# Kernel optimization log

Measured on AMD Instinct MI355X. Metric: run time of the kernel, lower is better.

The kernel has to match this reference:

```python
import jax, jax.numpy as jnp
import numpy as np

ALPHA = 1.0
BETA = 0.25
NUM_EMBEDS = 8192
EMBED_DIM = 512
B, T = 32, 256


def setup_inputs() -> dict:
    key = jax.random.key(0)
    k1, k2 = jax.random.split(key)
    z_e = jax.random.normal(k1, (B, EMBED_DIM, T), dtype=jnp.float32)
    codebook = jax.random.normal(k2, (NUM_EMBEDS, EMBED_DIM), dtype=jnp.float32)
    return {"z_e": z_e, "codebook": codebook}


def reference(z_e, codebook):
    # z_e: (b, d, t) -> (b, t, d)
    z = jnp.transpose(z_e, (0, 2, 1))
    b, t, d = z.shape
    flat = z.reshape(-1, d)  # (N, d), N = b*t

    # squared euclidean distances to every codebook vector: (N, K)
    dists = (
        jnp.sum(flat * flat, axis=1, keepdims=True)
        + jnp.sum(codebook * codebook, axis=1)
        - 2.0 * flat @ codebook.T
    )
    idx = jnp.argmin(dists, axis=1)  # (N,)

    # codebook lookup (equivalent to one-hot @ codebook)
    z_q = codebook[idx].reshape(b, t, d)

    # commitment loss (codebook is EMA-updated, so only e_latent term)
    e_latent_loss = jnp.mean((jax.lax.stop_gradient(z_q) - z) ** 2)
    vq_loss = ALPHA * BETA * e_latent_loss

    # straight-through estimator
    z_q_st = z + jax.lax.stop_gradient(z_q - z)
    z_q_out = jnp.transpose(z_q_st, (0, 2, 1))  # back to (b, d, t)

    # perplexity from mean one-hot assignment probabilities
    counts = jnp.zeros((codebook.shape[0],), dtype=jnp.float32).at[idx].add(1.0)
    avg_probs = counts / flat.shape[0]
    perplexity = jnp.exp(-jnp.sum(avg_probs * jnp.log(avg_probs + 1e-10)))

    return z_q_out, vq_loss, perplexity
```

## Files before the change

kernel.cpp:

```cpp
#include <hip/hip_runtime.h>
#include <stdint.h>

typedef _Float16 half8 __attribute__((ext_vector_type(8)));
typedef float floatx16 __attribute__((ext_vector_type(16)));
typedef unsigned long long u64;

#define ALPHA_ 1.0f
#define BETA_ 0.25f
#define NUM_EMBEDS 8192
#define EMBED_DIM 512
#define B_ 32
#define T_ 256
#define N_TOK 8192
#define MAXPAIRS (1 << 20)


__device__ __forceinline__ uint32_t mono(float s) {
    uint32_t u = __float_as_uint(s);
    return (u & 0x80000000u) ? ~u : (u | 0x80000000u);
}
__device__ __forceinline__ float unmono(uint32_t v) {
    return __uint_as_float((v & 0x80000000u) ? (v ^ 0x80000000u) : ~v);
}

__global__ void pack_cb_kernel(const float* __restrict__ cb, _Float16* __restrict__ cf,
                               float* __restrict__ cnorm, unsigned int* __restrict__ maxC2) {
    int row = blockIdx.x * 4 + (threadIdx.x >> 6);
    int l = threadIdx.x & 63;
    const float* src = cb + (size_t)row * EMBED_DIM + l * 8;
    float4 v0 = *(const float4*)src;
    float4 v1 = *(const float4*)(src + 4);
    float x[8] = {v0.x, v0.y, v0.z, v0.w, v1.x, v1.y, v1.z, v1.w};
    half8 hh;
    float s = 0.f;
#pragma unroll
    for (int j = 0; j < 8; ++j) {
        s += x[j] * x[j];
        hh[j] = (_Float16)x[j];
    }
    int slot = (l >> 2) * 2 + ((l >> 1) & 1);
    int flane = (row & 31) + (l & 1) * 32;
    *(half8*)(cf + (size_t)(row >> 5) * 16384 + (size_t)slot * 512 + flane * 8) = hh;
#pragma unroll
    for (int d = 32; d; d >>= 1) s += __shfl_xor(s, d, 64);
    if (l == 0) {
        cnorm[row] = s;
        atomicMax(maxC2, __float_as_uint(s));
    }
}

__global__ void pack_z_kernel(const float* __restrict__ z, _Float16* __restrict__ zf,
                              float* __restrict__ znorm) {
    int tid = threadIdx.x;
    int l = tid & 63, ds = tid >> 6;
    int n = blockIdx.x * 64 + l;
    int b = n >> 8, t = n & 255;
    int kk = ds >> 1, hfb = ds & 1;
    int tb = n >> 7, q = (n >> 5) & 3;
    size_t lanebase = (size_t)tb * 65536 + (size_t)q * 512 +
                      (size_t)((n & 31) + hfb * 32) * 8;
    float zz = 0.f;
    const int g0 = blockIdx.y * 4;
    for (int g = g0; g < g0 + 4; ++g) {
        int d0 = g * 32 + ds * 8;
        const float* src = z + ((size_t)b * EMBED_DIM + d0) * T_ + t;
        half8 hh;
#pragma unroll
        for (int j = 0; j < 8; ++j) {
            float zo = src[(size_t)j * T_];
            zz += zo * zo;
            hh[j] = (_Float16)(-2.0f * zo);
        }
        int slot = g * 2 + kk;
        *(half8*)(zf + lanebase + (size_t)slot * 2048) = hh;
    }
    atomicAdd(&znorm[n], zz);
}

#define MFMA16(a, b, c) __builtin_amdgcn_mfma_f32_32x32x16_f16(a, b, c, 0, 0, 0)

#define LDSET(s, hs)                                                  \
    fr[s][0] = *(const half8*)(Ab0 + (hs) * 512 + l8);                \
    fr[s][1] = *(const half8*)(Ab1 + (hs) * 512 + l8);                \
    fr[s][2] = *(const half8*)(Bb + (hs) * 2048 + 0 * 512 + l8);      \
    fr[s][3] = *(const half8*)(Bb + (hs) * 2048 + 1 * 512 + l8);      \
    fr[s][4] = *(const half8*)(Bb + (hs) * 2048 + 2 * 512 + l8);      \
    fr[s][5] = *(const half8*)(Bb + (hs) * 2048 + 3 * 512 + l8);

__global__ __launch_bounds__(256, 2) void argmin_kernel(
    const _Float16* __restrict__ cb_h, const _Float16* __restrict__ zt_h,
    const float* __restrict__ cnorm, u64* __restrict__ slot_m1,
    _Float16* __restrict__ slot_d) {
    const int tid = threadIdx.x;
    const int l = tid & 63;
    const int wv = tid >> 6;
    const int l31 = l & 31;
    const int hf = l >> 5;
    const int cid = blockIdx.y * 4 + wv;
    const _Float16* Ab0 = cb_h + (size_t)(cid * 2) * 16384;
    const _Float16* Ab1 = Ab0 + 16384;
    const _Float16* Bb = zt_h + (size_t)blockIdx.x * 65536;
    const int l8 = l * 8;

    floatx16 acc[2][4];
#pragma unroll
    for (int a = 0; a < 2; ++a)
#pragma unroll
        for (int q = 0; q < 4; ++q)
#pragma unroll
            for (int r = 0; r < 16; ++r) acc[a][q][r] = 0.f;

    half8 fr[3][6];
    LDSET(0, 0)
    LDSET(1, 1)
#pragma unroll
    for (int t = 0; t < 32; ++t) {
        const int s = t % 3;
        if ((t & 1) == 0) __syncthreads();
        if (t + 2 < 32) {
            LDSET((t + 2) % 3, t + 2)
        }
#pragma unroll
        for (int q = 0; q < 4; ++q) acc[0][q] = MFMA16(fr[s][0], fr[s][2 + q], acc[0][q]);
#pragma unroll
        for (int q = 0; q < 4; ++q) acc[1][q] = MFMA16(fr[s][1], fr[s][2 + q], acc[1][q]);
    }

    const int cb0 = cid * 64;
#pragma unroll
    for (int q = 0; q < 4; ++q) {
        u64 m1k = ~0ULL;
        float m1v = 3.4e38f, m2 = 3.4e38f;
#pragma unroll
        for (int ti = 0; ti < 2; ++ti)
#pragma unroll
            for (int g = 0; g < 4; ++g) {
                const int cb4 = cb0 + ti * 32 + g * 8 + hf * 4;
                float4 cn = *(const float4*)(cnorm + cb4);
                float sv[4] = {cn.x + acc[ti][q][g * 4 + 0], cn.y + acc[ti][q][g * 4 + 1],
                               cn.z + acc[ti][q][g * 4 + 2], cn.w + acc[ti][q][g * 4 + 3]};
#pragma unroll
                for (int r = 0; r < 4; ++r) {
                    u64 key = ((u64)mono(sv[r]) << 32) | (uint32_t)(cb4 + r);
                    if (key < m1k) { m2 = m1v; m1v = sv[r]; m1k = key; }
                    else m2 = fminf(m2, sv[r]);
                }
            }
        u64 ok = __shfl_xor(m1k, 32, 64);
        float ov = __shfl_xor(m1v, 32, 64);
        float om2 = __shfl_xor(m2, 32, 64);
        if (ok < m1k) { m2 = fminf(fminf(m2, om2), m1v); m1v = ov; m1k = ok; }
        else m2 = fminf(fminf(m2, om2), ov);
        if (hf == 0) {
            int tok = blockIdx.x * 128 + q * 32 + l31;
            slot_m1[((size_t)cid << 13) + tok] = m1k;
            slot_d[((size_t)cid << 13) + tok] = (_Float16)(m2 - m1v);
        }
    }
}

__global__ void combine_kernel(const u64* __restrict__ slot_m1, const _Float16* __restrict__ slot_d,
                               const float* __restrict__ znorm, const unsigned int* __restrict__ maxC2,
                               u64* __restrict__ wexact, int* __restrict__ pairs,
                               int* __restrict__ npairs) {
    int tid = threadIdx.x;
    int tok = blockIdx.x * 16 + (tid >> 4);
    int sub = tid & 15;
    u64 g1 = ~0ULL;
    float g1v = 3.4e38f, g2 = 3.4e38f;
    for (int c = sub; c < 128; c += 16) {
        u64 k = slot_m1[((size_t)c << 13) + tok];
        float kv = unmono((uint32_t)(k >> 32));
        float v2 = kv + (float)slot_d[((size_t)c << 13) + tok];
        if (k < g1) { g2 = fminf(g2, g1v); g1 = k; g1v = kv; }
        else g2 = fminf(g2, kv);
        g2 = fminf(g2, v2);
    }
#pragma unroll
    for (int m = 1; m < 16; m <<= 1) {
        u64 ok = __shfl_xor(g1, m, 64);
        float ov = __shfl_xor(g1v, m, 64);
        float o2 = __shfl_xor(g2, m, 64);
        if (ok < g1) { g2 = fminf(fminf(g2, o2), g1v); g1 = ok; g1v = ov; }
        else g2 = fminf(fminf(g2, o2), ov);
    }
    float maxC = sqrtf(__uint_as_float(*maxC2));
    float thr = sqrtf(znorm[tok]) * maxC * (1.0f / 256.0f) + 0.15f;
    if (g2 - g1v > thr) {
        if (sub == 0) wexact[tok] = g1;
    } else {
        float cutv = g1v + thr;
        for (int c = sub; c < 128; c += 16) {
            u64 k = slot_m1[((size_t)c << 13) + tok];
            if (unmono((uint32_t)(k >> 32)) <= cutv) {
                int i = atomicAdd(npairs, 1);
                if (i < MAXPAIRS) pairs[i] = (tok << 7) | c;
            }
        }
    }
}

__global__ void fallback_kernel(const float* __restrict__ z, const float* __restrict__ cb,
                                const float* __restrict__ cnorm,
                                const int* __restrict__ pairs, const int* __restrict__ npairs,
                                u64* __restrict__ wexact) {
    __shared__ float zs[4][512];
    int n = *npairs;
    if (n > MAXPAIRS) n = MAXPAIRS;
    const int l = threadIdx.x & 63, wv = threadIdx.x >> 6;
    int wid = blockIdx.x * 4 + wv;
    const int wstride = gridDim.x * 4;
    for (int pi = wid; pi < n; pi += wstride) {
        int pk = pairs[pi];
        int tok = pk >> 7, cid = pk & 127;
        int b = tok >> 8, t = tok & 255;
        const float* zp = z + (size_t)b * EMBED_DIM * T_ + t;
        float zv[8];
#pragma unroll
        for (int j = 0; j < 8; ++j) zv[j] = zp[(size_t)(l * 8 + j) * T_];
        *(float4*)&zs[wv][l * 8] = make_float4(zv[0], zv[1], zv[2], zv[3]);
        *(float4*)&zs[wv][l * 8 + 4] = make_float4(zv[4], zv[5], zv[6], zv[7]);
        int code = cid * 64 + l;
        const float* cp = cb + (size_t)code * EMBED_DIM;
        float acc = 0.f;
#pragma unroll 4
        for (int d = 0; d < 512; d += 4) {
            float4 cv = *(const float4*)(cp + d);
            float4 zq = *(const float4*)&zs[wv][d];
            acc += cv.x * zq.x + cv.y * zq.y + cv.z * zq.z + cv.w * zq.w;
        }
        float s = cnorm[code] - 2.0f * acc;
        u64 key = ((u64)mono(s) << 32) | (uint32_t)code;
#pragma unroll
        for (int m = 32; m; m >>= 1) {
            u64 ok = __shfl_xor(key, m, 64);
            key = ok < key ? ok : key;
        }
        if (l == 0) atomicMin(&wexact[tok], key);
    }
}

__global__ void gather_kernel(const float* __restrict__ z, const float* __restrict__ cb,
                              const u64* __restrict__ wexact,
                              float* __restrict__ out, int* __restrict__ counts,
                              float* __restrict__ sse_acc) {
    __shared__ unsigned int sIdx[32];
    __shared__ float red[16];
    const int tid = threadIdx.x;
    const int n0 = blockIdx.x * 32;
    const int b = n0 >> 8;
    const int t0 = n0 & 255;
    if (tid < 32) {
        unsigned int idx = (unsigned int)(wexact[n0 + tid] & 0xffffffffULL);
        sIdx[tid] = idx;
        atomicAdd(&counts[idx], 1);
    }
    __syncthreads();
    const int sg = tid >> 5;
    const int l32 = tid & 31;
    const float* crow = cb + (size_t)sIdx[l32] * EMBED_DIM;
    const size_t base = ((size_t)b * EMBED_DIM) * T_ + (size_t)(t0 + l32);
    float sse = 0.f;
    const int d0 = sg * 32;
#pragma unroll 8
    for (int i = 0; i < 32; ++i) {
        int d = d0 + i;
        float v = crow[d];
        size_t o = base + (size_t)d * T_;
        float diff = v - z[o];
        out[o] = v;
        sse += diff * diff;
    }
#pragma unroll
    for (int m = 16; m; m >>= 1) sse += __shfl_xor(sse, m, 64);
    if (l32 == 0) red[sg] = sse;
    __syncthreads();
    if (tid == 0) {
        float s = 0.f;
#pragma unroll
        for (int i = 0; i < 16; ++i) s += red[i];
        atomicAdd(sse_acc, s);
    }
}

__global__ void finalize_kernel(const int* __restrict__ counts,
                                const float* __restrict__ sse_acc,
                                float* __restrict__ out) {
    __shared__ float red[4];
    const int tid = threadIdx.x;
    float e = 0.f;
    for (int k = tid; k < NUM_EMBEDS; k += 256) {
        float p = (float)counts[k] * (1.0f / (float)N_TOK);
        e += p * logf(p + 1e-10f);
    }
    for (int m = 32; m; m >>= 1) e += __shfl_xor(e, m, 64);
    if ((tid & 63) == 0) red[tid >> 6] = e;
    __syncthreads();
    if (tid == 0) {
        float ent = red[0] + red[1] + red[2] + red[3];
        size_t off = (size_t)B_ * EMBED_DIM * T_;
        out[off + 0] = (ALPHA_ * BETA_) * sse_acc[0] / (float)((size_t)N_TOK * EMBED_DIM);
        out[off + 1] = expf(-ent);
    }
}

extern "C" void kernel_launch(void* const* d_in, const int* in_sizes, int n_in,
                              void* d_out, int out_size, void* d_ws, size_t ws_size,
                              hipStream_t stream) {
    const float* z = (const float*)d_in[0];
    const float* cb = (const float*)d_in[1];
    float* out = (float*)d_out;
    char* ws = (char*)d_ws;
    u64* wexact = (u64*)ws;
    float* cnorm = (float*)(ws + 65536);
    int* counts = (int*)(ws + 98304);
    float* znorm = (float*)(ws + 131072);
    float* sse = (float*)(ws + 163840);
    int* npairs = (int*)(ws + 163844);
    unsigned int* maxC2 = (unsigned int*)(ws + 163848);
    u64* slot_m1 = (u64*)(ws + (1ull << 20));
    _Float16* slot_d = (_Float16*)(ws + (9ull << 20));
    _Float16* cb_h = (_Float16*)(ws + (10ull << 20));
    _Float16* zt_h = (_Float16*)(ws + (18ull << 20));
    int* pairs = (int*)(ws + (26ull << 20));

    hipMemsetAsync(wexact, 0xFF, NUM_EMBEDS * sizeof(u64), stream);
    hipMemsetAsync(counts, 0, 65536 + 12, stream);

    pack_cb_kernel<<<NUM_EMBEDS / 4, 256, 0, stream>>>(cb, cb_h, cnorm, maxC2);
    pack_z_kernel<<<dim3(N_TOK / 64, 4), 256, 0, stream>>>(z, zt_h, znorm);
    argmin_kernel<<<dim3(N_TOK / 128, 32), 256, 0, stream>>>(cb_h, zt_h, cnorm, slot_m1, slot_d);
    combine_kernel<<<N_TOK / 16, 256, 0, stream>>>(slot_m1, slot_d, znorm, maxC2, wexact, pairs, npairs);
    fallback_kernel<<<512, 256, 0, stream>>>(z, cb, cnorm, pairs, npairs, wexact);
    gather_kernel<<<N_TOK / 32, 512, 0, stream>>>(z, cb, wexact, out, counts, sse);
    finalize_kernel<<<1, 256, 0, stream>>>(counts, sse, out);
}
```

Measured before the change: 426.3 us.

## Stage argmin GEMM tiles through LDS, widen code tiles, fuse pack and fallback kernels

Result: slower. 516.9 us (+21.2%).

```diff
diff --git a/kernel.cpp b/kernel.cpp
--- a/kernel.cpp
+++ b/kernel.cpp
@@ -12,7 +12,6 @@
 #define B_ 32
 #define T_ 256
 #define N_TOK 8192
-#define MAXPAIRS (1 << 20)
 
 
 __device__ __forceinline__ uint32_t mono(float s) {
@@ -23,116 +22,152 @@
     return __uint_as_float((v & 0x80000000u) ? (v ^ 0x80000000u) : ~v);
 }
 
-__global__ void pack_cb_kernel(const float* __restrict__ cb, _Float16* __restrict__ cf,
-                               float* __restrict__ cnorm, unsigned int* __restrict__ maxC2) {
-    int row = blockIdx.x * 4 + (threadIdx.x >> 6);
-    int l = threadIdx.x & 63;
-    const float* src = cb + (size_t)row * EMBED_DIM + l * 8;
-    float4 v0 = *(const float4*)src;
-    float4 v1 = *(const float4*)(src + 4);
-    float x[8] = {v0.x, v0.y, v0.z, v0.w, v1.x, v1.y, v1.z, v1.w};
-    half8 hh;
-    float s = 0.f;
-#pragma unroll
-    for (int j = 0; j < 8; ++j) {
-        s += x[j] * x[j];
-        hh[j] = (_Float16)x[j];
-    }
-    int slot = (l >> 2) * 2 + ((l >> 1) & 1);
-    int flane = (row & 31) + (l & 1) * 32;
-    *(half8*)(cf + (size_t)(row >> 5) * 16384 + (size_t)slot * 512 + flane * 8) = hh;
-#pragma unroll
-    for (int d = 32; d; d >>= 1) s += __shfl_xor(s, d, 64);
-    if (l == 0) {
-        cnorm[row] = s;
-        atomicMax(maxC2, __float_as_uint(s));
-    }
-}
-
-__global__ void pack_z_kernel(const float* __restrict__ z, _Float16* __restrict__ zf,
-                              float* __restrict__ znorm) {
+__global__ void pack_kernel(const float* __restrict__ cb, const float* __restrict__ z,
+                            _Float16* __restrict__ cf, _Float16* __restrict__ zf,
+                            float* __restrict__ cnorm, unsigned int* __restrict__ maxC2,
+                            float* __restrict__ znorm) {
     int tid = threadIdx.x;
-    int l = tid & 63, ds = tid >> 6;
-    int n = blockIdx.x * 64 + l;
-    int b = n >> 8, t = n & 255;
-    int kk = ds >> 1, hfb = ds & 1;
-    int tb = n >> 7, q = (n >> 5) & 3;
-    size_t lanebase = (size_t)tb * 65536 + (size_t)q * 512 +
-                      (size_t)((n & 31) + hfb * 32) * 8;
-    float zz = 0.f;
-    const int g0 = blockIdx.y * 4;
-    for (int g = g0; g < g0 + 4; ++g) {
-        int d0 = g * 32 + ds * 8;
-        const float* src = z + ((size_t)b * EMBED_DIM + d0) * T_ + t;
+    if (blockIdx.x < 2048) {
+        int row = blockIdx.x * 4 + (tid >> 6);
+        int l = tid & 63;
+        const float* src = cb + (size_t)row * EMBED_DIM + l * 8;
+        float4 v0 = *(const float4*)src;
+        float4 v1 = *(const float4*)(src + 4);
+        float x[8] = {v0.x, v0.y, v0.z, v0.w, v1.x, v1.y, v1.z, v1.w};
         half8 hh;
+        float s = 0.f;
 #pragma unroll
         for (int j = 0; j < 8; ++j) {
-            float zo = src[(size_t)j * T_];
-            zz += zo * zo;
-            hh[j] = (_Float16)(-2.0f * zo);
-        }
-        int slot = g * 2 + kk;
-        *(half8*)(zf + lanebase + (size_t)slot * 2048) = hh;
-    }
-    atomicAdd(&znorm[n], zz);
+            s += x[j] * x[j];
+            hh[j] = (_Float16)x[j];
+        }
+        int slot = (l >> 2) * 2 + ((l >> 1) & 1);
+        int flane = (row & 31) + (l & 1) * 32;
+        *(half8*)(cf + (size_t)(row >> 5) * 16384 + (size_t)slot * 512 + flane * 8) = hh;
+#pragma unroll
+        for (int d = 32; d; d >>= 1) s += __shfl_xor(s, d, 64);
+        if (l == 0) {
+            cnorm[row] = s;
+            atomicMax(maxC2, __float_as_uint(s));
+        }
+    } else {
+        int zb = blockIdx.x - 2048;
+        int bx = zb & 127, g0 = (zb >> 7) * 4;
+        int l = tid & 63, ds = tid >> 6;
+        int n = bx * 64 + l;
+        int b = n >> 8, t = n & 255;
+        int kk = ds >> 1, hfb = ds & 1;
+        int tb = n >> 7, q = (n >> 5) & 3;
+        size_t lanebase = (size_t)tb * 65536 + (size_t)q * 512 +
+                          (size_t)((n & 31) + hfb * 32) * 8;
+        float zz = 0.f;
+        for (int g = g0; g < g0 + 4; ++g) {
+            int d0 = g * 32 + ds * 8;
+            const float* src = z + ((size_t)b * EMBED_DIM + d0) * T_ + t;
+            half8 hh;
+#pragma unroll
+            for (int j = 0; j < 8; ++j) {
+                float zo = src[(size_t)j * T_];
+                zz += zo * zo;
+                hh[j] = (_Float16)(-2.0f * zo);
+            }
+            int slot = g * 2 + kk;
+            *(half8*)(zf + lanebase + (size_t)slot * 2048) = hh;
+        }
+        atomicAdd(&znorm[n], zz);
+    }
 }
 
 #define MFMA16(a, b, c) __builtin_amdgcn_mfma_f32_32x32x16_f16(a, b, c, 0, 0, 0)
-
-#define LDSET(s, hs)                                                  \
-    fr[s][0] = *(const half8*)(Ab0 + (hs) * 512 + l8);                \
-    fr[s][1] = *(const half8*)(Ab1 + (hs) * 512 + l8);                \
-    fr[s][2] = *(const half8*)(Bb + (hs) * 2048 + 0 * 512 + l8);      \
-    fr[s][3] = *(const half8*)(Bb + (hs) * 2048 + 1 * 512 + l8);      \
-    fr[s][4] = *(const half8*)(Bb + (hs) * 2048 + 2 * 512 + l8);      \
-    fr[s][5] = *(const half8*)(Bb + (hs) * 2048 + 3 * 512 + l8);
 
 __global__ __launch_bounds__(256, 2) void argmin_kernel(
     const _Float16* __restrict__ cb_h, const _Float16* __restrict__ zt_h,
     const float* __restrict__ cnorm, u64* __restrict__ slot_m1,
     _Float16* __restrict__ slot_d) {
+    __shared__ alignas(16) _Float16 Sm[2][12288];
     const int tid = threadIdx.x;
     const int l = tid & 63;
     const int wv = tid >> 6;
     const int l31 = l & 31;
     const int hf = l >> 5;
-    const int cid = blockIdx.y * 4 + wv;
-    const _Float16* Ab0 = cb_h + (size_t)(cid * 2) * 16384;
-    const _Float16* Ab1 = Ab0 + 16384;
-    const _Float16* Bb = zt_h + (size_t)blockIdx.x * 65536;
+    const int wm = wv >> 1;
+    const int wn = wv & 1;
     const int l8 = l * 8;
 
-    floatx16 acc[2][4];
-#pragma unroll
-    for (int a = 0; a < 2; ++a)
-#pragma unroll
-        for (int q = 0; q < 4; ++q)
+    const int flat = blockIdx.y * gridDim.x + blockIdx.x;
+    const int cpx = (gridDim.x * gridDim.y) >> 3;
+    const int swz = (flat & 7) * cpx + (flat >> 3);
+    const int tb = swz & 63;
+    const int cg = swz >> 6;
+    const int c0 = cg * 256;
+
+    const _Float16* Abase = cb_h + (size_t)(cg * 8) * 16384;
+    const _Float16* Bbase = zt_h + (size_t)tb * 65536;
+
+    floatx16 acc[4][2];
+#pragma unroll
+    for (int a = 0; a < 4; ++a)
+#pragma unroll
+        for (int q = 0; q < 2; ++q)
 #pragma unroll
             for (int r = 0; r < 16; ++r) acc[a][q][r] = 0.f;
 
-    half8 fr[3][6];
-    LDSET(0, 0)
-    LDSET(1, 1)
-#pragma unroll
-    for (int t = 0; t < 32; ++t) {
-        const int s = t % 3;
-        if ((t & 1) == 0) __syncthreads();
-        if (t + 2 < 32) {
-            LDSET((t + 2) % 3, t + 2)
-        }
-#pragma unroll
-        for (int q = 0; q < 4; ++q) acc[0][q] = MFMA16(fr[s][0], fr[s][2 + q], acc[0][q]);
-#pragma unroll
-        for (int q = 0; q < 4; ++q) acc[1][q] = MFMA16(fr[s][1], fr[s][2 + q], acc[1][q]);
-    }
-
-    const int cb0 = cid * 64;
-#pragma unroll
-    for (int q = 0; q < 4; ++q) {
+    half8 sa[4], sb[2];
+    auto load_stage = [&](int t) {
+#pragma unroll
+        for (int i = 0; i < 4; ++i) {
+            int j = wv * 4 + i;
+            sa[i] = *(const half8*)(Abase + (size_t)(j >> 1) * 16384 +
+                                    (size_t)(2 * t + (j & 1)) * 512 + l8);
+        }
+#pragma unroll
+        for (int i = 0; i < 2; ++i) {
+            int jb = wv * 2 + i;
+            sb[i] = *(const half8*)(Bbase + (size_t)(2 * t + (jb >> 2)) * 2048 +
+                                    (size_t)(jb & 3) * 512 + l8);
+        }
+    };
+    auto write_stage = [&](int p) {
+        _Float16* dst = Sm[p];
+#pragma unroll
+        for (int i = 0; i < 4; ++i)
+            *(half8*)(dst + (wv * 4 + i) * 512 + l8) = sa[i];
+#pragma unroll
+        for (int i = 0; i < 2; ++i)
+            *(half8*)(dst + 8192 + (wv * 2 + i) * 512 + l8) = sb[i];
+    };
+
+    load_stage(0);
+    write_stage(0);
+    __syncthreads();
+    for (int t = 0; t < 16; ++t) {
+        const int p = t & 1;
+        if (t < 15) load_stage(t + 1);
+        const _Float16* Ab = Sm[p] + (size_t)(wm * 8) * 512;
+        const _Float16* Bb = Sm[p] + 8192 + (size_t)wn * 1024;
+#pragma unroll
+        for (int kk = 0; kk < 2; ++kk) {
+            half8 b0 = *(const half8*)(Bb + kk * 2048 + l8);
+            half8 b1 = *(const half8*)(Bb + kk * 2048 + 512 + l8);
+#pragma unroll
+            for (int ti = 0; ti < 4; ++ti) {
+                half8 a = *(const half8*)(Ab + (size_t)(ti * 2 + kk) * 512 + l8);
+                acc[ti][0] = MFMA16(a, b0, acc[ti][0]);
+                acc[ti][1] = MFMA16(a, b1, acc[ti][1]);
+            }
+        }
+        if (t < 15) write_stage(p ^ 1);
+        __syncthreads();
+    }
+
+    const int cb0 = c0 + wm * 128;
+    const int cid = cg * 2 + wm;
+#pragma unroll
+    for (int q = 0; q < 2; ++q) {
         u64 m1k = ~0ULL;
         float m1v = 3.4e38f, m2 = 3.4e38f;
 #pragma unroll
-        for (int ti = 0; ti < 2; ++ti)
+        for (int ti = 0; ti < 4; ++ti)
 #pragma unroll
             for (int g = 0; g < 4; ++g) {
                 const int cb4 = cb0 + ti * 32 + g * 8 + hf * 4;
@@ -152,23 +187,29 @@
         if (ok < m1k) { m2 = fminf(fminf(m2, om2), m1v); m1v = ov; m1k = ok; }
         else m2 = fminf(fminf(m2, om2), ov);
         if (hf == 0) {
-            int tok = blockIdx.x * 128 + q * 32 + l31;
+            int tok = tb * 128 + wn * 64 + q * 32 + l31;
             slot_m1[((size_t)cid << 13) + tok] = m1k;
             slot_d[((size_t)cid << 13) + tok] = (_Float16)(m2 - m1v);
         }
     }
 }
 
-__global__ void combine_kernel(const u64* __restrict__ slot_m1, const _Float16* __restrict__ slot_d,
-                               const float* __restrict__ znorm, const unsigned int* __restrict__ maxC2,
-                               u64* __restrict__ wexact, int* __restrict__ pairs,
-                               int* __restrict__ npairs) {
-    int tid = threadIdx.x;
-    int tok = blockIdx.x * 16 + (tid >> 4);
-    int sub = tid & 15;
+__global__ void combinefb_kernel(const u64* __restrict__ slot_m1, const _Float16* __restrict__ slot_d,
+                                 const float* __restrict__ znorm, const unsigned int* __restrict__ maxC2,
+                                 const float* __restrict__ z, const float* __restrict__ cb,
+                                 const float* __restrict__ cnorm, u64* __restrict__ wexact) {
+    __shared__ unsigned short sPair[1024];
+    __shared__ int snp;
+    __shared__ float zs[4][512];
+    const int tid = threadIdx.x;
+    if (tid == 0) snp = 0;
+    __syncthreads();
+
+    const int ti16 = tid >> 4, sub = tid & 15;
+    const int tok = blockIdx.x * 16 + ti16;
     u64 g1 = ~0ULL;
     float g1v = 3.4e38f, g2 = 3.4e38f;
-    for (int c = sub; c < 128; c += 16) {
+    for (int c = sub; c < 64; c += 16) {
         u64 k = slot_m1[((size_t)c << 13) + tok];
         float kv = unmono((uint32_t)(k >> 32));
         float v2 = kv + (float)slot_d[((size_t)c << 13) + tok];
@@ -190,53 +231,50 @@
         if (sub == 0) wexact[tok] = g1;
     } else {
         float cutv = g1v + thr;
-        for (int c = sub; c < 128; c += 16) {
+        for (int c = sub; c < 64; c += 16) {
             u64 k = slot_m1[((size_t)c << 13) + tok];
             if (unmono((uint32_t)(k >> 32)) <= cutv) {
-                int i = atomicAdd(npairs, 1);
-                if (i < MAXPAIRS) pairs[i] = (tok << 7) | c;
-            }
-        }
-    }
-}
-
-__global__ void fallback_kernel(const float* __restrict__ z, const float* __restrict__ cb,
-                                const float* __restrict__ cnorm,
-                                const int* __restrict__ pairs, const int* __restrict__ npairs,
-                                u64* __restrict__ wexact) {
-    __shared__ float zs[4][512];
-    int n = *npairs;
-    if (n > MAXPAIRS) n = MAXPAIRS;
-    const int l = threadIdx.x & 63, wv = threadIdx.x >> 6;
-    int wid = blockIdx.x * 4 + wv;
-    const int wstride = gridDim.x * 4;
-    for (int pi = wid; pi < n; pi += wstride) {
-        int pk = pairs[pi];
-        int tok = pk >> 7, cid = pk & 127;
-        int b = tok >> 8, t = tok & 255;
+                int i = atomicAdd(&snp, 1);
+                sPair[i] = (unsigned short)((ti16 << 6) | c);
+            }
+        }
+    }
+    __syncthreads();
+
+    const int np = snp;
+    const int l = tid & 63, wv = tid >> 6;
+    for (int p = wv; p < np; p += 4) {
+        int pk = sPair[p];
+        int tk = blockIdx.x * 16 + (pk >> 6), cid = pk & 63;
+        int b = tk >> 8, t = tk & 255;
         const float* zp = z + (size_t)b * EMBED_DIM * T_ + t;
         float zv[8];
 #pragma unroll
         for (int j = 0; j < 8; ++j) zv[j] = zp[(size_t)(l * 8 + j) * T_];
         *(float4*)&zs[wv][l * 8] = make_float4(zv[0], zv[1], zv[2], zv[3]);
         *(float4*)&zs[wv][l * 8 + 4] = make_float4(zv[4], zv[5], zv[6], zv[7]);
-        int code = cid * 64 + l;
-        const float* cp = cb + (size_t)code * EMBED_DIM;
-        float acc = 0.f;
+        u64 best = ~0ULL;
+#pragma unroll
+        for (int jj = 0; jj < 2; ++jj) {
+            int code = cid * 128 + jj * 64 + l;
+            const float* cp = cb + (size_t)code * EMBED_DIM;
+            float acc = 0.f;
 #pragma unroll 4
-        for (int d = 0; d < 512; d += 4) {
-            float4 cv = *(const float4*)(cp + d);
-            float4 zq = *(const float4*)&zs[wv][d];
-            acc += cv.x * zq.x + cv.y * zq.y + cv.z * zq.z + cv.w * zq.w;
-        }
-        float s = cnorm[code] - 2.0f * acc;
-        u64 key = ((u64)mono(s) << 32) | (uint32_t)code;
+            for (int d = 0; d < 512; d += 4) {
+                float4 cv = *(const float4*)(cp + d);
+                float4 zq = *(const float4*)&zs[wv][d];
+                acc += cv.x * zq.x + cv.y * zq.y + cv.z * zq.z + cv.w * zq.w;
+            }
+            float s = cnorm[code] - 2.0f * acc;
+            u64 key = ((u64)mono(s) << 32) | (uint32_t)code;
+            if (key < best) best = key;
+        }
 #pragma unroll
         for (int m = 32; m; m >>= 1) {
-            u64 ok = __shfl_xor(key, m, 64);
-            key = ok < key ? ok : key;
-        }
-        if (l == 0) atomicMin(&wexact[tok], key);
+            u64 ok = __shfl_xor(best, m, 64);
+            best = ok < best ? ok : best;
+        }
+        if (l == 0) atomicMin(&wexact[tk], best);
     }
 }
 
@@ -316,22 +354,18 @@
     int* counts = (int*)(ws + 98304);
     float* znorm = (float*)(ws + 131072);
     float* sse = (float*)(ws + 163840);
-    int* npairs = (int*)(ws + 163844);
     unsigned int* maxC2 = (unsigned int*)(ws + 163848);
     u64* slot_m1 = (u64*)(ws + (1ull << 20));
-    _Float16* slot_d = (_Float16*)(ws + (9ull << 20));
-    _Float16* cb_h = (_Float16*)(ws + (10ull << 20));
-    _Float16* zt_h = (_Float16*)(ws + (18ull << 20));
-    int* pairs = (int*)(ws + (26ull << 20));
+    _Float16* slot_d = (_Float16*)(ws + (5ull << 20));
+    _Float16* cb_h = (_Float16*)(ws + (6ull << 20));
+    _Float16* zt_h = (_Float16*)(ws + (14ull << 20));
 
     hipMemsetAsync(wexact, 0xFF, NUM_EMBEDS * sizeof(u64), stream);
     hipMemsetAsync(counts, 0, 65536 + 12, stream);
 
-    pack_cb_kernel<<<NUM_EMBEDS / 4, 256, 0, stream>>>(cb, cb_h, cnorm, maxC2);
-    pack_z_kernel<<<dim3(N_TOK / 64, 4), 256, 0, stream>>>(z, zt_h, znorm);
-    argmin_kernel<<<dim3(N_TOK / 128, 32), 256, 0, stream>>>(cb_h, zt_h, cnorm, slot_m1, slot_d);
-    combine_kernel<<<N_TOK / 16, 256, 0, stream>>>(slot_m1, slot_d, znorm, maxC2, wexact, pairs, npairs);
-    fallback_kernel<<<512, 256, 0, stream>>>(z, cb, cnorm, pairs, npairs, wexact);
+    pack_kernel<<<2560, 256, 0, stream>>>(cb, z, cb_h, zt_h, cnorm, maxC2, znorm);
+    argmin_kernel<<<dim3(64, 32), 256, 0, stream>>>(cb_h, zt_h, cnorm, slot_m1, slot_d);
+    combinefb_kernel<<<N_TOK / 16, 256, 0, stream>>>(slot_m1, slot_d, znorm, maxC2, z, cb, cnorm, wexact);
     gather_kernel<<<N_TOK / 32, 512, 0, stream>>>(z, cb, wexact, out, counts, sse);
     finalize_kernel<<<1, 256, 0, stream>>>(counts, sse, out);
 }
```
